# Optimization experiments

Hardware: AMD Instinct MI355X
Metric: run time of the kernel (lower is better)

## Reference

```python
import jax, jax.numpy as jnp
import numpy as np

B, N, D, H, MLP = 4, 1024, 1024, 16, 4096  # seq_len N must equal dim D; D = H * dim_head
DH = D // H
EPS = 1e-5


def layernorm(x, g, b):
    mu = jnp.mean(x, axis=-1, keepdims=True)
    var = jnp.var(x, axis=-1, keepdims=True)
    return (x - mu) * jax.lax.rsqrt(var + EPS) * g + b


def setup_inputs() -> dict:
    key = jax.random.key(0)
    ks = jax.random.split(key, 12)
    s = 0.02
    return {
        "x": jax.random.normal(ks[0], (B, N, D), jnp.float32),
        "enc_out": jax.random.normal(ks[1], (B, N, D), jnp.float32),
        # SelfAttention (heads=1, dim_head=D); weights stored (in, out) so we apply x @ W
        "sa_wq": jax.random.normal(ks[2], (D, D), jnp.float32) * s,
        "sa_wk": jax.random.normal(ks[3], (D, D), jnp.float32) * s,
        "sa_wv": jax.random.normal(ks[4], (D, D), jnp.float32) * s,
        "sa_g": jnp.ones((D,), jnp.float32),
        "sa_b": jnp.zeros((D,), jnp.float32),
        # CrossAttention
        "ca_wq": jax.random.normal(ks[5], (D, D), jnp.float32) * s,
        "ca_wk": jax.random.normal(ks[6], (D, D), jnp.float32) * s,
        "ca_wv": jax.random.normal(ks[7], (D, D), jnp.float32) * s,
        "ca_g": jnp.ones((D,), jnp.float32),
        "ca_b": jnp.zeros((D,), jnp.float32),
        # FeedForward
        "w1": jax.random.normal(ks[8], (D, MLP), jnp.float32) * s,
        "b1": jnp.zeros((MLP,), jnp.float32),
        "w2": jax.random.normal(ks[9], (MLP, D), jnp.float32) * s,
        "b2": jnp.zeros((D,), jnp.float32),
        "ff_g": jnp.ones((D,), jnp.float32),
        "ff_b": jnp.zeros((D,), jnp.float32),
    }


def reference(x, enc_out, sa_wq, sa_wk, sa_wv, sa_g, sa_b,
              ca_wq, ca_wk, ca_wv, ca_g, ca_b,
              w1, b1, w2, b2, ff_g, ff_b):
    b, n, d = x.shape
    # --- SelfAttention: heads=1, dim_head=dim -> scale = dim**-0.5 ---
    sa_scale = 1.0 / jnp.sqrt(jnp.asarray(d, x.dtype))
    q = x @ sa_wq
    k = x @ sa_wk
    v = x @ sa_wv
    dots = jnp.einsum('bid,bjd->bij', q, k) * sa_scale
    attn = jax.nn.softmax(dots, axis=-1)
    sa = jnp.einsum('bij,bjd->bid', attn, v)
    sa = layernorm(sa + x, sa_g, sa_b)

    # --- CrossAttention: Q . (K K^T) before softmax ---
    dh = d // H
    ca_scale = 1.0 / jnp.sqrt(jnp.asarray(dh, x.dtype))
    qc = sa @ ca_wq                                     # [b, n, d]; broadcast over heads
    kc = (enc_out @ ca_wk).reshape(b, n, H, dh).transpose(0, 2, 1, 3)  # [b, h, n, dh]
    vc = (enc_out @ ca_wv).reshape(b, n, H, dh).transpose(0, 2, 1, 3)
    kkt = jnp.einsum('bhid,bhjd->bhij', kc, kc) * ca_scale             # [b, h, n, n]
    dots = jnp.einsum('bid,bhjd->bhij', qc, kkt) * ca_scale            # q's d contracts kkt's last dim (n == d)
    attn = jax.nn.softmax(dots, axis=-1)
    out = jnp.einsum('bhij,bhjd->bhid', attn, vc)
    out = out.transpose(0, 2, 1, 3).reshape(b, n, d)
    ca = layernorm(out + enc_out, ca_g, ca_b)

    # --- FeedForward (dropout = identity in eval) ---
    h = jax.nn.gelu(ca @ w1 + b1, approximate=False) @ w2 + b2
    return layernorm(h + ca, ff_g, ff_b)
```

## Files before the change

### kernel.cpp

```cpp
#include <hip/hip_runtime.h>
#include <math.h>
#include <stdint.h>

typedef unsigned short u16;
typedef u16   u16x8 __attribute__((ext_vector_type(8)));
typedef __bf16 bf16x8 __attribute__((ext_vector_type(8)));
typedef float  f32x4 __attribute__((ext_vector_type(4)));

#define B_   4
#define N_   1024
#define D_   1024
#define MLP_ 4096

__device__ __forceinline__ float bf2f(u16 v) {
    unsigned u = ((unsigned)v) << 16;
    return __builtin_bit_cast(float, u);
}
__device__ __forceinline__ u16 f2bf(float f) {
    unsigned u = __builtin_bit_cast(unsigned, f);
    u += 0x7fff + ((u >> 16) & 1);
    return (u16)(u >> 16);
}
__device__ __forceinline__ bf16x8 ld8(const u16* p) {
    return __builtin_bit_cast(bf16x8, *(const u16x8*)p);
}
__device__ __forceinline__ void gll16(const u16* g, u16* l) {
    __builtin_amdgcn_global_load_lds(
        (const __attribute__((address_space(1))) unsigned int*)g,
        (__attribute__((address_space(3))) unsigned int*)l,
        16, 0, 0);
}

__global__ __launch_bounds__(256)
void f32_to_bf16_k(const float* __restrict__ in, u16* __restrict__ out, int n8)
{
    int i = blockIdx.x * 256 + threadIdx.x;
    if (i < n8) {
        f32x4 a = *(const f32x4*)&in[(long)i * 8];
        f32x4 b = *(const f32x4*)&in[(long)i * 8 + 4];
        u16x8 h;
        h[0] = f2bf(a[0]); h[1] = f2bf(a[1]); h[2] = f2bf(a[2]); h[3] = f2bf(a[3]);
        h[4] = f2bf(b[0]); h[5] = f2bf(b[1]); h[6] = f2bf(b[2]); h[7] = f2bf(b[3]);
        *(u16x8*)&out[(long)i * 8] = h;
    }
}

template<int TM, int TN, int OUTF32, int BIAS, int GELU>
__global__ __launch_bounds__(256, 4)
void gemm_a(const u16* __restrict__ A, const u16* __restrict__ Bt,
            void* __restrict__ Cv, const float* __restrict__ bias,
            float scale, int K,
            int lda, int ldb, int ldc,
            long sA, long sB, long sC)
{
    constexpr int MT = TM / 32, NT = TN / 32;
    __shared__ alignas(16) u16 As[2][TM * 32];
    __shared__ alignas(16) u16 Bs[2][TN * 32];
    const int bz = blockIdx.z;
    A  += bz * sA;  Bt += bz * sB;
    char* Cp = (char*)Cv + bz * sC * (OUTF32 ? 4 : 2);
    const int m0 = blockIdx.x * TM, n0 = blockIdx.y * TN;
    const int t = threadIdx.x, lane = t & 63, w = t >> 6;
    const int wr = (w >> 1) * (TM / 2), wc = (w & 1) * (TN / 2);
    const int fr = lane & 15, fq = lane >> 4, fk = fq * 8;
    f32x4 acc[MT][NT] = {};

    const int r0a = t >> 2, c0a = (t & 3) * 8;
    auto stageA = [&](u16* dst, int k0) {
#pragma unroll
        for (int p = 0; p < TM / 64; p++)
            gll16(A + (long)(m0 + p * 64 + r0a) * lda + k0 + c0a, dst + p * 2048 + w * 512);
    };
    auto stageB = [&](u16* dst, int k0) {
#pragma unroll
        for (int p = 0; p < TN / 64; p++)
            gll16(Bt + (long)(n0 + p * 64 + r0a) * ldb + k0 + c0a, dst + p * 2048 + w * 512);
    };

    stageA(As[0], 0);
    stageB(Bs[0], 0);
    int cur = 0;
    for (int k0 = 0; k0 < K; k0 += 32) {
        __syncthreads();
        if (k0 + 32 < K) {
            stageA(As[cur ^ 1], k0 + 32);
            stageB(Bs[cur ^ 1], k0 + 32);
        }
        const u16* as = As[cur];
        const u16* bs = Bs[cur];
        bf16x8 af[MT], bfv[NT];
#pragma unroll
        for (int mt = 0; mt < MT; mt++) af [mt] = ld8(&as[(wr + mt * 16 + fr) * 32 + fk]);
#pragma unroll
        for (int nt = 0; nt < NT; nt++) bfv[nt] = ld8(&bs[(wc + nt * 16 + fr) * 32 + fk]);
#pragma unroll
        for (int mt = 0; mt < MT; mt++)
#pragma unroll
            for (int nt = 0; nt < NT; nt++)
                acc[mt][nt] = __builtin_amdgcn_mfma_f32_16x16x32_bf16(af[mt], bfv[nt], acc[mt][nt], 0, 0, 0);
        cur ^= 1;
    }

#pragma unroll
    for (int nt = 0; nt < NT; nt++) {
        const int col = n0 + wc + nt * 16 + fr;
        float bv = 0.f;
        if (BIAS) bv = bias[col];
#pragma unroll
        for (int mt = 0; mt < MT; mt++) {
            const int rbase = m0 + wr + mt * 16 + fq * 4;
#pragma unroll
            for (int r = 0; r < 4; r++) {
                float v = acc[mt][nt][r] * scale;
                if (BIAS) v += bv;
                if (GELU) v = 0.5f * v * (1.0f + erff(v * 0.70710678118654752f));
                long idx = (long)(rbase + r) * ldc + col;
                if (OUTF32) ((float*)Cp)[idx] = v;
                else        ((u16*) Cp)[idx] = f2bf(v);
            }
        }
    }
}

template<int INF32>
__global__ __launch_bounds__(256)
void transpose_cast(const void* __restrict__ in, u16* __restrict__ out,
                    int R, int C, long sIn, long sOut)
{
    __shared__ u16 tile[32][33];
    const char* ip = (const char*)in + (long)blockIdx.z * sIn * (INF32 ? 4 : 2);
    u16*        op = out + (long)blockIdx.z * sOut;
    const int bx = blockIdx.x * 32, by = blockIdx.y * 32;
    const int tx = threadIdx.x & 31, ty = threadIdx.x >> 5;
#pragma unroll
    for (int i = ty; i < 32; i += 8) {
        long idx = (long)(by + i) * C + bx + tx;
        tile[i][tx] = INF32 ? f2bf(((const float*)ip)[idx]) : ((const u16*)ip)[idx];
    }
    __syncthreads();
#pragma unroll
    for (int i = ty; i < 32; i += 8) op[(long)(bx + i) * R + by + tx] = tile[tx][i];
}

__global__ __launch_bounds__(256)
void softmax_1024(const float* __restrict__ in, u16* __restrict__ out)
{
    const int lane = threadIdx.x & 63, wv = threadIdx.x >> 6;
    const long row = (long)blockIdx.x * 4 + wv;
    const float* p = in + row * 1024;
    float v[16], mx = -1e30f;
#pragma unroll
    for (int i = 0; i < 16; i++) { v[i] = p[lane + i * 64]; mx = fmaxf(mx, v[i]); }
#pragma unroll
    for (int off = 32; off; off >>= 1) mx = fmaxf(mx, __shfl_xor(mx, off, 64));
    float s = 0.f;
#pragma unroll
    for (int i = 0; i < 16; i++) { v[i] = __expf(v[i] - mx); s += v[i]; }
#pragma unroll
    for (int off = 32; off; off >>= 1) s += __shfl_xor(s, off, 64);
    const float inv = 1.0f / s;
    u16* q = out + row * 1024;
#pragma unroll
    for (int i = 0; i < 16; i++) q[lane + i * 64] = f2bf(v[i] * inv);
}

template<int AF32, int RESF32, int OUTF32>
__global__ __launch_bounds__(256)
void ln_res(const void* __restrict__ Av, const void* __restrict__ Rv,
            const float* __restrict__ g, const float* __restrict__ be,
            void* __restrict__ out)
{
    const int lane = threadIdx.x & 63, wv = threadIdx.x >> 6;
    const long row = (long)blockIdx.x * 4 + wv;
    float v[16], s = 0.f;
#pragma unroll
    for (int i = 0; i < 16; i++) {
        long idx = row * 1024 + lane + i * 64;
        float a = AF32   ? ((const float*)Av)[idx] : bf2f(((const u16*)Av)[idx]);
        float r = RESF32 ? ((const float*)Rv)[idx] : bf2f(((const u16*)Rv)[idx]);
        v[i] = a + r;
        s += v[i];
    }
#pragma unroll
    for (int off = 32; off; off >>= 1) s += __shfl_xor(s, off, 64);
    const float mu = s * (1.f / 1024.f);
    float s2 = 0.f;
#pragma unroll
    for (int i = 0; i < 16; i++) { float d = v[i] - mu; s2 += d * d; }
#pragma unroll
    for (int off = 32; off; off >>= 1) s2 += __shfl_xor(s2, off, 64);
    const float rs = rsqrtf(s2 * (1.f / 1024.f) + 1e-5f);
#pragma unroll
    for (int i = 0; i < 16; i++) {
        int c = lane + i * 64;
        float o = (v[i] - mu) * rs * g[c] + be[c];
        if (OUTF32) ((float*)out)[row * 1024 + c] = o;
        else        ((u16*) out)[row * 1024 + c] = f2bf(o);
    }
}

__global__ __launch_bounds__(256, 3)
void flash_ca(const u16* __restrict__ P, const u16* __restrict__ Kc,
              const u16* __restrict__ VT, u16* __restrict__ O)
{
    __shared__ alignas(16) u16 Ks[2][64 * 64];
    __shared__ alignas(16) u16 Vs[2][64 * 64];
    __shared__ alignas(16) u16 Ps[128 * 72];
    const int b = blockIdx.z, h = blockIdx.y, it = blockIdx.x;
    const long base = (long)b * N_ * D_;
    const int t = threadIdx.x, lane = t & 63, w = t >> 6;
    const int fr = lane & 15, fq = lane >> 4;

    bf16x8 qf[2][2];
#pragma unroll
    for (int mt = 0; mt < 2; mt++)
#pragma unroll
        for (int hf = 0; hf < 2; hf++)
            qf[mt][hf] = ld8(&P[base + (long)(it * 128 + w * 32 + mt * 16 + fr) * D_
                                + h * 64 + hf * 32 + fq * 8]);

    auto stageK = [&](int buf, int jt) {
#pragma unroll
        for (int p = 0; p < 2; p++)
            gll16(Kc + base + (long)(jt * 64 + p * 32 + (t >> 3)) * D_ + h * 64 + (t & 7) * 8,
                  &Ks[buf][p * 2048 + w * 512]);
    };
    auto stageV = [&](int buf, int jt) {
#pragma unroll
        for (int p = 0; p < 2; p++)
            gll16(VT + base + (long)(h * 64 + p * 32 + (t >> 3)) * D_ + jt * 64 + (t & 7) * 8,
                  &Vs[buf][p * 2048 + w * 512]);
    };

    f32x4 o[2][4] = {};
    float l_lane[2][4] = {};

    stageK(0, 0); stageV(0, 0);
    int cur = 0;
    for (int jt = 0; jt < 16; jt++) {
        __syncthreads();
        if (jt + 1 < 16) { stageK(cur ^ 1, jt + 1); stageV(cur ^ 1, jt + 1); }
        const u16* ks = Ks[cur];
        const u16* vs = Vs[cur];

        f32x4 st[2][4] = {};
#pragma unroll
        for (int nt = 0; nt < 4; nt++) {
            bf16x8 b0 = ld8(&ks[(nt * 16 + fr) * 64 + fq * 8]);
            bf16x8 b1 = ld8(&ks[(nt * 16 + fr) * 64 + 32 + fq * 8]);
#pragma unroll
            for (int mt = 0; mt < 2; mt++) {
                st[mt][nt] = __builtin_amdgcn_mfma_f32_16x16x32_bf16(qf[mt][0], b0, st[mt][nt], 0, 0, 0);
                st[mt][nt] = __builtin_amdgcn_mfma_f32_16x16x32_bf16(qf[mt][1], b1, st[mt][nt], 0, 0, 0);
            }
        }
#pragma unroll
        for (int mt = 0; mt < 2; mt++)
#pragma unroll
            for (int nt = 0; nt < 4; nt++)
#pragma unroll
                for (int r = 0; r < 4; r++) {
                    float e = __expf(st[mt][nt][r]);
                    l_lane[mt][r] += e;
                    Ps[(w * 32 + mt * 16 + fq * 4 + r) * 72 + nt * 16 + fr] = f2bf(e);
                }
        __asm__ volatile("s_waitcnt lgkmcnt(0)" ::: "memory");
        bf16x8 vf[4][2];
#pragma unroll
        for (int dt = 0; dt < 4; dt++) {
            vf[dt][0] = ld8(&vs[(dt * 16 + fr) * 64 + fq * 8]);
            vf[dt][1] = ld8(&vs[(dt * 16 + fr) * 64 + 32 + fq * 8]);
        }
#pragma unroll
        for (int mt = 0; mt < 2; mt++) {
            bf16x8 p0 = ld8(&Ps[(w * 32 + mt * 16 + fr) * 72 + fq * 8]);
            bf16x8 p1 = ld8(&Ps[(w * 32 + mt * 16 + fr) * 72 + 32 + fq * 8]);
#pragma unroll
            for (int dt = 0; dt < 4; dt++) {
                o[mt][dt] = __builtin_amdgcn_mfma_f32_16x16x32_bf16(p0, vf[dt][0], o[mt][dt], 0, 0, 0);
                o[mt][dt] = __builtin_amdgcn_mfma_f32_16x16x32_bf16(p1, vf[dt][1], o[mt][dt], 0, 0, 0);
            }
        }
        cur ^= 1;
    }
#pragma unroll
    for (int mt = 0; mt < 2; mt++)
#pragma unroll
        for (int r = 0; r < 4; r++) {
            float lt = l_lane[mt][r];
#pragma unroll
            for (int off = 1; off < 16; off <<= 1) lt += __shfl_xor(lt, off, 64);
            l_lane[mt][r] = 1.0f / lt;
        }
#pragma unroll
    for (int mt = 0; mt < 2; mt++)
#pragma unroll
        for (int dt = 0; dt < 4; dt++)
#pragma unroll
            for (int r = 0; r < 4; r++)
                O[base + (long)(it * 128 + w * 32 + mt * 16 + fq * 4 + r) * D_
                  + h * 64 + dt * 16 + fr] = f2bf(o[mt][dt][r] * l_lane[mt][r]);
}

extern "C" void kernel_launch(void* const* d_in, const int* in_sizes, int n_in,
                              void* d_out, int out_size, void* d_ws, size_t ws_size,
                              hipStream_t stream)
{
    const float* x     = (const float*)d_in[0];
    const float* enc   = (const float*)d_in[1];
    const float* sa_wq = (const float*)d_in[2];
    const float* sa_wk = (const float*)d_in[3];
    const float* sa_wv = (const float*)d_in[4];
    const float* sa_g  = (const float*)d_in[5];
    const float* sa_b  = (const float*)d_in[6];
    const float* ca_wq = (const float*)d_in[7];
    const float* ca_wk = (const float*)d_in[8];
    const float* ca_wv = (const float*)d_in[9];
    const float* ca_g  = (const float*)d_in[10];
    const float* ca_b  = (const float*)d_in[11];
    const float* w1    = (const float*)d_in[12];
    const float* b1    = (const float*)d_in[13];
    const float* w2    = (const float*)d_in[14];
    const float* b2    = (const float*)d_in[15];
    const float* ff_g  = (const float*)d_in[16];
    const float* ff_b  = (const float*)d_in[17];

    char* ws = (char*)d_ws;
    const size_t MB = 1ull << 20;
    u16*  qkB   = (u16*)(ws + 0 * MB);
    u16*  E     = (u16*)(ws + 0 * MB);
    u16*  h1B   = (u16*)(ws + 0 * MB);
    float* scF  = (float*)(ws + 16 * MB);
    u16*  xB    = (u16*)(ws + 32 * MB);
    u16*  encB  = (u16*)(ws + 40 * MB);
    float* h2F  = (float*)(ws + 32 * MB);
    u16*  Wsa   = (u16*)(ws + 48 * MB);
    u16*  qB    = (u16*)(ws + 48 * MB);
    u16*  calnB = (u16*)(ws + 48 * MB);
    u16*  kB    = (u16*)(ws + 56 * MB);
    u16*  w2T   = (u16*)(ws + 56 * MB);
    u16*  vTB   = (u16*)(ws + 64 * MB);
    u16*  w1T   = (u16*)(ws + 64 * MB);
    u16*  attnB = (u16*)(ws + 72 * MB);
    u16*  Wca   = (u16*)(ws + 72 * MB);

    const dim3 blk(256, 1, 1);
    const long M1 = (long)N_ * D_;
    const long M2 = 2 * M1;

    f32_to_bf16_k<<<dim3(2048, 1, 1), blk, 0, stream>>>(x,   xB,   524288);
    f32_to_bf16_k<<<dim3(2048, 1, 1), blk, 0, stream>>>(enc, encB, 524288);

    transpose_cast<1><<<dim3(32, 32, 1), blk, 0, stream>>>(sa_wq, Wsa,          1024, 1024, 0, 0);
    transpose_cast<1><<<dim3(32, 32, 1), blk, 0, stream>>>(sa_wk, Wsa + M1,     1024, 1024, 0, 0);
    transpose_cast<1><<<dim3(32, 32, 1), blk, 0, stream>>>(sa_wv, Wsa + 2 * M1, 1024, 1024, 0, 0);

    gemm_a<64,128,0,0,0><<<dim3(64, 16, 1), blk, 0, stream>>>(xB, Wsa, qkB, nullptr,
        1.f, 1024, 1024, 1024, 2048, 0, 0, 0);
    gemm_a<64,64,0,0,0><<<dim3(16, 16, 4), blk, 0, stream>>>(Wsa + 2 * M1, xB, vTB, nullptr,
        1.f, 1024, 1024, 1024, 1024, 0, M1, M1);
    gemm_a<64,64,1,0,0><<<dim3(16, 16, 4), blk, 0, stream>>>(qkB, qkB + 1024, scF, nullptr,
        0.03125f, 1024, 2048, 2048, 1024, M2, M2, M1);
    softmax_1024<<<dim3(1024, 1, 1), blk, 0, stream>>>(scF, attnB);
    gemm_a<64,64,1,0,0><<<dim3(16, 16, 4), blk, 0, stream>>>(attnB, vTB, scF, nullptr,
        1.f, 1024, 1024, 1024, 1024, M1, M1, M1);
    ln_res<1,1,0><<<dim3(1024, 1, 1), blk, 0, stream>>>(scF, x, sa_g, sa_b, E);

    transpose_cast<1><<<dim3(32, 32, 1), blk, 0, stream>>>(ca_wq, Wca,          1024, 1024, 0, 0);
    transpose_cast<1><<<dim3(32, 32, 1), blk, 0, stream>>>(ca_wk, Wca + M1,     1024, 1024, 0, 0);
    transpose_cast<1><<<dim3(32, 32, 1), blk, 0, stream>>>(ca_wv, Wca + 2 * M1, 1024, 1024, 0, 0);
    gemm_a<64,64,0,0,0><<<dim3(64, 16, 1), blk, 0, stream>>>(E, Wca, qB, nullptr,
        1.f, 1024, 1024, 1024, 1024, 0, 0, 0);
    gemm_a<64,64,0,0,0><<<dim3(64, 16, 1), blk, 0, stream>>>(encB, Wca + M1, kB, nullptr,
        1.f, 1024, 1024, 1024, 1024, 0, 0, 0);
    gemm_a<64,64,0,0,0><<<dim3(16, 16, 4), blk, 0, stream>>>(Wca + 2 * M1, encB, vTB, nullptr,
        1.f, 1024, 1024, 1024, 1024, 0, M1, M1);
    transpose_cast<0><<<dim3(32, 32, 4), blk, 0, stream>>>(kB, E, 1024, 1024, M1, M1);
    gemm_a<64,64,0,0,0><<<dim3(16, 16, 4), blk, 0, stream>>>(qB, E, attnB, nullptr,
        0.015625f, 1024, 1024, 1024, 1024, M1, M1, M1);
    flash_ca<<<dim3(8, 16, 4), blk, 0, stream>>>(attnB, kB, vTB, E);
    ln_res<0,1,0><<<dim3(1024, 1, 1), blk, 0, stream>>>(E, enc, ca_g, ca_b, calnB);

    transpose_cast<1><<<dim3(128, 32, 1), blk, 0, stream>>>(w1, w1T, 1024, 4096, 0, 0);
    transpose_cast<1><<<dim3(32, 128, 1), blk, 0, stream>>>(w2, w2T, 4096, 1024, 0, 0);
    gemm_a<128,128,0,1,1><<<dim3(32, 32, 1), blk, 0, stream>>>(calnB, w1T, h1B, b1,
        1.f, 1024, 1024, 1024, 4096, 0, 0, 0);
    gemm_a<64,64,1,1,0><<<dim3(64, 16, 1), blk, 0, stream>>>(h1B, w2T, h2F, b2,
        1.f, 4096, 4096, 4096, 1024, 0, 0, 0);
    ln_res<1,0,1><<<dim3(1024, 1, 1), blk, 0, stream>>>(h2F, calnB, ff_g, ff_b, (float*)d_out);
}
```

Before: 543.8 us.

## Batch paired GEMMs into single launches and enlarge GEMM tiles

Adds a SEL template mode to the GEMM so one launch can serve two independent problems, chosen by splitting grid y or z. Self-attention Q/K, both V projections, and cross-attention Q/K each run as one combined launch. Most GEMMs move from 64x64 to 128x64 or 128x128 tiles, with launch bounds lowered to 3 for large tiles, and the workspace buffers are re-laid out so both V projections can live side by side. The goal is fewer kernel launches, fewer tail waves and more operand reuse per tile, at the cost of fewer resident blocks per CU and a riskier buffer aliasing plan.

```diff
diff --git a/kernel.cpp b/kernel.cpp
--- a/kernel.cpp
+++ b/kernel.cpp
@@ -45,10 +45,12 @@
     }
 }
 
-template<int TM, int TN, int OUTF32, int BIAS, int GELU>
-__global__ __launch_bounds__(256, 4)
-void gemm_a(const u16* __restrict__ A, const u16* __restrict__ Bt,
-            void* __restrict__ Cv, const float* __restrict__ bias,
+template<int TM, int TN, int SEL, int OUTF32, int BIAS, int GELU>
+__global__ __launch_bounds__(256, (TM + TN >= 256) ? 3 : 4)
+void gemm_a(const u16* __restrict__ A0, const u16* __restrict__ A1,
+            const u16* __restrict__ B0, const u16* __restrict__ B1,
+            void* __restrict__ C0v, void* __restrict__ C1v,
+            const float* __restrict__ bias,
             float scale, int K,
             int lda, int ldb, int ldc,
             long sA, long sB, long sC)
@@ -56,10 +58,18 @@
     constexpr int MT = TM / 32, NT = TN / 32;
     __shared__ alignas(16) u16 As[2][TM * 32];
     __shared__ alignas(16) u16 Bs[2][TN * 32];
-    const int bz = blockIdx.z;
-    A  += bz * sA;  Bt += bz * sB;
-    char* Cp = (char*)Cv + bz * sC * (OUTF32 ? 4 : 2);
-    const int m0 = blockIdx.x * TM, n0 = blockIdx.y * TN;
+    int by = blockIdx.y, bz = blockIdx.z;
+    const u16* A = A0; const u16* Bt = B0; char* Cp = (char*)C0v;
+    if (SEL == 1) {
+        int half = gridDim.y >> 1;
+        if (by >= half) { A = A1; Bt = B1; Cp = (char*)C1v; by -= half; }
+    }
+    if (SEL == 2) {
+        int half = gridDim.z >> 1;
+        if (bz >= half) { A = A1; Bt = B1; Cp = (char*)C1v; bz -= half; }
+    }
+    A += bz * sA;  Bt += bz * sB;  Cp += bz * sC * (OUTF32 ? 4 : 2);
+    const int m0 = blockIdx.x * TM, n0 = by * TN;
     const int t = threadIdx.x, lane = t & 63, w = t >> 6;
     const int wr = (w >> 1) * (TM / 2), wc = (w & 1) * (TN / 2);
     const int fr = lane & 15, fq = lane >> 4, fk = fq * 8;
@@ -327,65 +337,72 @@
 
     char* ws = (char*)d_ws;
     const size_t MB = 1ull << 20;
-    u16*  qkB   = (u16*)(ws + 0 * MB);
-    u16*  E     = (u16*)(ws + 0 * MB);
-    u16*  h1B   = (u16*)(ws + 0 * MB);
-    float* scF  = (float*)(ws + 16 * MB);
-    u16*  xB    = (u16*)(ws + 32 * MB);
-    u16*  encB  = (u16*)(ws + 40 * MB);
-    float* h2F  = (float*)(ws + 32 * MB);
-    u16*  Wsa   = (u16*)(ws + 48 * MB);
-    u16*  qB    = (u16*)(ws + 48 * MB);
-    u16*  calnB = (u16*)(ws + 48 * MB);
-    u16*  kB    = (u16*)(ws + 56 * MB);
-    u16*  w2T   = (u16*)(ws + 56 * MB);
-    u16*  vTB   = (u16*)(ws + 64 * MB);
-    u16*  w1T   = (u16*)(ws + 64 * MB);
-    u16*  attnB = (u16*)(ws + 72 * MB);
-    u16*  Wca   = (u16*)(ws + 72 * MB);
+    u16*  xB    = (u16*)(ws + 0 * MB);
+    u16*  attnB = (u16*)(ws + 0 * MB);
+    u16*  w2T   = (u16*)(ws + 0 * MB);
+    u16*  encB  = (u16*)(ws + 8 * MB);
+    u16*  w1T   = (u16*)(ws + 8 * MB);
+    u16*  Wsa   = (u16*)(ws + 16 * MB);
+    u16*  Wca   = (u16*)(ws + 22 * MB);
+    float* h2F  = (float*)(ws + 16 * MB);
+    u16*  qBsa  = (u16*)(ws + 28 * MB);
+    u16*  E     = (u16*)(ws + 28 * MB);
+    u16*  kBsa  = (u16*)(ws + 36 * MB);
+    u16*  qBca  = (u16*)(ws + 36 * MB);
+    u16*  calnB = (u16*)(ws + 36 * MB);
+    u16*  vTB   = (u16*)(ws + 44 * MB);
+    u16*  kBca  = (u16*)(ws + 44 * MB);
+    u16*  h1B   = (u16*)(ws + 44 * MB);
+    u16*  vcTB  = (u16*)(ws + 52 * MB);
+    float* scF  = (float*)(ws + 60 * MB);
+    u16*  kcT   = (u16*)(ws + 60 * MB);
 
     const dim3 blk(256, 1, 1);
     const long M1 = (long)N_ * D_;
-    const long M2 = 2 * M1;
+    const long W1M = (long)1024 * 1024;
 
     f32_to_bf16_k<<<dim3(2048, 1, 1), blk, 0, stream>>>(x,   xB,   524288);
     f32_to_bf16_k<<<dim3(2048, 1, 1), blk, 0, stream>>>(enc, encB, 524288);
 
-    transpose_cast<1><<<dim3(32, 32, 1), blk, 0, stream>>>(sa_wq, Wsa,          1024, 1024, 0, 0);
-    transpose_cast<1><<<dim3(32, 32, 1), blk, 0, stream>>>(sa_wk, Wsa + M1,     1024, 1024, 0, 0);
-    transpose_cast<1><<<dim3(32, 32, 1), blk, 0, stream>>>(sa_wv, Wsa + 2 * M1, 1024, 1024, 0, 0);
-
-    gemm_a<64,128,0,0,0><<<dim3(64, 16, 1), blk, 0, stream>>>(xB, Wsa, qkB, nullptr,
-        1.f, 1024, 1024, 1024, 2048, 0, 0, 0);
-    gemm_a<64,64,0,0,0><<<dim3(16, 16, 4), blk, 0, stream>>>(Wsa + 2 * M1, xB, vTB, nullptr,
+    transpose_cast<1><<<dim3(32, 32, 1), blk, 0, stream>>>(sa_wq, Wsa,           1024, 1024, 0, 0);
+    transpose_cast<1><<<dim3(32, 32, 1), blk, 0, stream>>>(sa_wk, Wsa + W1M,     1024, 1024, 0, 0);
+    transpose_cast<1><<<dim3(32, 32, 1), blk, 0, stream>>>(sa_wv, Wsa + 2 * W1M, 1024, 1024, 0, 0);
+    transpose_cast<1><<<dim3(32, 32, 1), blk, 0, stream>>>(ca_wq, Wca,           1024, 1024, 0, 0);
+    transpose_cast<1><<<dim3(32, 32, 1), blk, 0, stream>>>(ca_wk, Wca + W1M,     1024, 1024, 0, 0);
+    transpose_cast<1><<<dim3(32, 32, 1), blk, 0, stream>>>(ca_wv, Wca + 2 * W1M, 1024, 1024, 0, 0);
+
+    gemm_a<128,128,1,0,0,0><<<dim3(32, 16, 1), blk, 0, stream>>>(
+        xB, xB, Wsa, Wsa + W1M, qBsa, kBsa, nullptr,
+        1.f, 1024, 1024, 1024, 1024, 0, 0, 0);
+    gemm_a<128,128,2,0,0,0><<<dim3(8, 8, 8), blk, 0, stream>>>(
+        Wsa + 2 * W1M, Wca + 2 * W1M, xB, encB, vTB, vcTB, nullptr,
         1.f, 1024, 1024, 1024, 1024, 0, M1, M1);
-    gemm_a<64,64,1,0,0><<<dim3(16, 16, 4), blk, 0, stream>>>(qkB, qkB + 1024, scF, nullptr,
-        0.03125f, 1024, 2048, 2048, 1024, M2, M2, M1);
+    gemm_a<128,64,0,1,0,0><<<dim3(8, 16, 4), blk, 0, stream>>>(
+        qBsa, nullptr, kBsa, nullptr, scF, nullptr, nullptr,
+        0.03125f, 1024, 1024, 1024, 1024, M1, M1, M1);
     softmax_1024<<<dim3(1024, 1, 1), blk, 0, stream>>>(scF, attnB);
-    gemm_a<64,64,1,0,0><<<dim3(16, 16, 4), blk, 0, stream>>>(attnB, vTB, scF, nullptr,
+    gemm_a<128,64,0,1,0,0><<<dim3(8, 16, 4), blk, 0, stream>>>(
+        attnB, nullptr, vTB, nullptr, scF, nullptr, nullptr,
         1.f, 1024, 1024, 1024, 1024, M1, M1, M1);
     ln_res<1,1,0><<<dim3(1024, 1, 1), blk, 0, stream>>>(scF, x, sa_g, sa_b, E);
 
-    transpose_cast<1><<<dim3(32, 32, 1), blk, 0, stream>>>(ca_wq, Wca,          1024, 1024, 0, 0);
-    transpose_cast<1><<<dim3(32, 32, 1), blk, 0, stream>>>(ca_wk, Wca + M1,     1024, 1024, 0, 0);
-    transpose_cast<1><<<dim3(32, 32, 1), blk, 0, stream>>>(ca_wv, Wca + 2 * M1, 1024, 1024, 0, 0);
-    gemm_a<64,64,0,0,0><<<dim3(64, 16, 1), blk, 0, stream>>>(E, Wca, qB, nullptr,
+    gemm_a<128,128,1,0,0,0><<<dim3(32, 16, 1), blk, 0, stream>>>(
+        E, encB, Wca, Wca + W1M, qBca, kBca, nullptr,
         1.f, 1024, 1024, 1024, 1024, 0, 0, 0);
-    gemm_a<64,64,0,0,0><<<dim3(64, 16, 1), blk, 0, stream>>>(encB, Wca + M1, kB, nullptr,
-        1.f, 1024, 1024, 1024, 1024, 0, 0, 0);
-    gemm_a<64,64,0,0,0><<<dim3(16, 16, 4), blk, 0, stream>>>(Wca + 2 * M1, encB, vTB, nullptr,
-        1.f, 1024, 1024, 1024, 1024, 0, M1, M1);
-    transpose_cast<0><<<dim3(32, 32, 4), blk, 0, stream>>>(kB, E, 1024, 1024, M1, M1);
-    gemm_a<64,64,0,0,0><<<dim3(16, 16, 4), blk, 0, stream>>>(qB, E, attnB, nullptr,
+    transpose_cast<0><<<dim3(32, 32, 4), blk, 0, stream>>>(kBca, kcT, 1024, 1024, M1, M1);
+    gemm_a<128,64,0,0,0,0><<<dim3(8, 16, 4), blk, 0, stream>>>(
+        qBca, nullptr, kcT, nullptr, attnB, nullptr, nullptr,
         0.015625f, 1024, 1024, 1024, 1024, M1, M1, M1);
-    flash_ca<<<dim3(8, 16, 4), blk, 0, stream>>>(attnB, kB, vTB, E);
+    flash_ca<<<dim3(8, 16, 4), blk, 0, stream>>>(attnB, kBca, vcTB, E);
     ln_res<0,1,0><<<dim3(1024, 1, 1), blk, 0, stream>>>(E, enc, ca_g, ca_b, calnB);
 
     transpose_cast<1><<<dim3(128, 32, 1), blk, 0, stream>>>(w1, w1T, 1024, 4096, 0, 0);
     transpose_cast<1><<<dim3(32, 128, 1), blk, 0, stream>>>(w2, w2T, 4096, 1024, 0, 0);
-    gemm_a<128,128,0,1,1><<<dim3(32, 32, 1), blk, 0, stream>>>(calnB, w1T, h1B, b1,
+    gemm_a<128,128,0,0,1,1><<<dim3(32, 32, 1), blk, 0, stream>>>(
+        calnB, nullptr, w1T, nullptr, h1B, nullptr, b1,
         1.f, 1024, 1024, 1024, 4096, 0, 0, 0);
-    gemm_a<64,64,1,1,0><<<dim3(64, 16, 1), blk, 0, stream>>>(h1B, w2T, h2F, b2,
+    gemm_a<128,64,0,1,1,0><<<dim3(32, 16, 1), blk, 0, stream>>>(
+        h1B, nullptr, w2T, nullptr, h2F, nullptr, b2,
         1.f, 4096, 4096, 4096, 1024, 0, 0, 0);
     ln_res<1,0,1><<<dim3(1024, 1, 1), blk, 0, stream>>>(h2F, calnB, ff_g, ff_b, (float*)d_out);
 }
```

New measurement: 525.4 us. -3.4%, faster.
